# Kernel tuning notes

Hardware: AMD Instinct MI355X
Metric: run time of the kernel (lower is better)

## Reference

```python
import jax, jax.numpy as jnp
import numpy as np

EPS_W = 1e-8   # weight reciprocal eps (matches torch code)
EPS_BN = 1e-5  # torch BatchNorm1d default eps


def _cdist(a, b):
    # a: [B,N,3], b: [B,M,3] -> [B,N,M] euclidean distances
    sq = (jnp.sum(a * a, -1)[:, :, None] + jnp.sum(b * b, -1)[:, None, :]
          - 2.0 * jnp.einsum('bnd,bmd->bnm', a, b))
    return jnp.sqrt(jnp.maximum(sq, 0.0))


def _bn_relu(x, gamma, beta):
    # x: [B,C,N]; training-mode batch norm over (B,N)
    mean = jnp.mean(x, axis=(0, 2), keepdims=True)
    var = jnp.mean((x - mean) ** 2, axis=(0, 2), keepdims=True)
    y = (x - mean) * jax.lax.rsqrt(var + EPS_BN)
    y = y * gamma[None, :, None] + beta[None, :, None]
    return jax.nn.relu(y)


def setup_inputs() -> dict:
    key = jax.random.key(0)
    ks = jax.random.split(key, 8)
    B, Np, Ns = 16, 1024, 4096
    Cp, Cs, Co = 256, 128, 256
    return {
        'xyz_prev': jax.random.normal(ks[0], (B, Np, 3), jnp.float32),
        'xyz_skip': jax.random.normal(ks[1], (B, Ns, 3), jnp.float32),
        'points_prev': jax.random.normal(ks[2], (B, Cp, Np), jnp.float32),
        'points_skip': jax.random.normal(ks[3], (B, Cs, Ns), jnp.float32),
        'W1': jax.random.normal(ks[4], (Co, Cp + Cs), jnp.float32) * 0.05,
        'g1': jnp.ones((Co,), jnp.float32),
        'b1': jnp.zeros((Co,), jnp.float32),
        'W2': jax.random.normal(ks[5], (Co, Co), jnp.float32) * 0.05,
        'g2': jnp.ones((Co,), jnp.float32),
        'b2': jnp.zeros((Co,), jnp.float32),
    }


def reference(xyz_prev, xyz_skip, points_prev, points_skip, W1, g1, b1, W2, g2, b2):
    dist = _cdist(xyz_skip, xyz_prev)                       # [B,Ns,Np]
    neg, idx = jax.lax.top_k(-dist, 3)                      # 3 smallest dists
    dist_recip = 1.0 / (dist + EPS_W)
    # NOTE: normalization is over ALL N_prev points (faithful to source)
    weight = dist_recip / jnp.sum(dist_recip, axis=2, keepdims=True)
    w3 = jnp.take_along_axis(weight, idx, axis=2)           # [B,Ns,3]
    pp = jnp.swapaxes(points_prev, 1, 2)                    # [B,Np,Cp]
    g = jnp.take_along_axis(pp[:, None, :, :], idx[..., None], axis=2)  # [B,Ns,3,Cp]
    interp = jnp.einsum('bnk,bnkc->bcn', w3, g)             # [B,Cp,Ns]
    x = jnp.concatenate([interp, points_skip], axis=1)      # [B,Cp+Cs,Ns]
    x = _bn_relu(jnp.einsum('bcn,oc->bon', x, W1), g1, b1)
    x = _bn_relu(jnp.einsum('bcn,oc->bon', x, W2), g2, b2)
    return x
```

## Files before the change

### kernel.cpp

```cpp
#include <hip/hip_runtime.h>
#include <math.h>

constexpr int NB  = 16;
constexpr int NP  = 1024;
constexpr int NS  = 4096;
constexpr int CP  = 256;
constexpr int CS  = 128;
constexpr int CIN = 384;
constexpr int CO  = 256;

constexpr int NCHUNK = 16;
constexpr int CHPTS  = NP / NCHUNK;

typedef unsigned int uint;
typedef unsigned short ushort_t;
typedef __attribute__((ext_vector_type(8))) short short8;
typedef __attribute__((ext_vector_type(8))) unsigned short us8;
typedef __attribute__((ext_vector_type(4))) float f32x4;

__device__ __forceinline__ ushort_t f2bf(float f) {
  uint u = __float_as_uint(f);
  uint r = (u + 0x7fffu + ((u >> 16) & 1u)) >> 16;
  return (ushort_t)r;
}
__device__ __forceinline__ float bf2f(ushort_t u) {
  return __uint_as_float(((uint)u) << 16);
}

__device__ __forceinline__ void gload16(const void* g, void* l) {
  __builtin_amdgcn_global_load_lds(
      (const __attribute__((address_space(1))) uint*)g,
      (__attribute__((address_space(3))) uint*)l, 16, 0, 0);
}

__device__ __forceinline__ void tkp(float pxv, float pyv, float pzv, int pi,
                                    float qx, float qy, float qz,
                                    float& k0, float& k1, float& k2,
                                    float& rsum) {
  float dx = pxv - qx, dy = pyv - qy, dz = pzv - qz;
  float sq = fmaf(dz, dz, fmaf(dy, dy, fmaf(dx, dx, 1e-16f)));
  rsum += __builtin_amdgcn_rsqf(sq);
  float k = __uint_as_float((__float_as_uint(sq) & 0xFFFFFC00u) | (uint)pi);
  k2 = __builtin_amdgcn_fmed3f(k1, k2, k);
  k1 = __builtin_amdgcn_fmed3f(k0, k1, k);
  k0 = fminf(k0, k);
}

__global__ __launch_bounds__(256) void topk_chunk_kernel(
    const float* __restrict__ xyz_prev, const float* __restrict__ xyz_skip,
    float* __restrict__ pbuf) {
  __shared__ float px[CHPTS], py[CHPTS], pz[CHPTS];
  int q  = blockIdx.y;
  int b  = blockIdx.z;
  int tid = threadIdx.x;
  if (tid < CHPTS) {
    const float* xp = xyz_prev + ((size_t)b * NP + q * CHPTS + tid) * 3;
    px[tid] = xp[0]; py[tid] = xp[1]; pz[tid] = xp[2];
  }
  __syncthreads();
  int nA = blockIdx.x * 512 + tid;
  int nB = nA + 256;
  const float* xqA = xyz_skip + ((size_t)b * NS + nA) * 3;
  const float* xqB = xyz_skip + ((size_t)b * NS + nB) * 3;
  float qxA = xqA[0], qyA = xqA[1], qzA = xqA[2];
  float qxB = xqB[0], qyB = xqB[1], qzB = xqB[2];
  float kA0 = INFINITY, kA1 = INFINITY, kA2 = INFINITY;
  float kB0 = INFINITY, kB1 = INFINITY, kB2 = INFINITY;
  float rsA = 0.f, rsB = 0.f;
  int pbase = q * CHPTS;
  for (int p = 0; p < CHPTS; p += 4) {
    float4 X = *(const float4*)&px[p];
    float4 Y = *(const float4*)&py[p];
    float4 Z = *(const float4*)&pz[p];
    tkp(X.x, Y.x, Z.x, pbase + p + 0, qxA, qyA, qzA, kA0, kA1, kA2, rsA);
    tkp(X.x, Y.x, Z.x, pbase + p + 0, qxB, qyB, qzB, kB0, kB1, kB2, rsB);
    tkp(X.y, Y.y, Z.y, pbase + p + 1, qxA, qyA, qzA, kA0, kA1, kA2, rsA);
    tkp(X.y, Y.y, Z.y, pbase + p + 1, qxB, qyB, qzB, kB0, kB1, kB2, rsB);
    tkp(X.z, Y.z, Z.z, pbase + p + 2, qxA, qyA, qzA, kA0, kA1, kA2, rsA);
    tkp(X.z, Y.z, Z.z, pbase + p + 2, qxB, qyB, qzB, kB0, kB1, kB2, rsB);
    tkp(X.w, Y.w, Z.w, pbase + p + 3, qxA, qyA, qzA, kA0, kA1, kA2, rsA);
    tkp(X.w, Y.w, Z.w, pbase + p + 3, qxB, qyB, qzB, kB0, kB1, kB2, rsB);
  }
  size_t PA = ((size_t)(b * NCHUNK + q) * NS + nA) * 4;
  size_t PB = ((size_t)(b * NCHUNK + q) * NS + nB) * 4;
  *(float4*)(pbuf + PA) = make_float4(kA0, kA1, kA2, rsA);
  *(float4*)(pbuf + PB) = make_float4(kB0, kB1, kB2, rsB);
}

__global__ __launch_bounds__(256) void topk_merge_kernel(
    const float* __restrict__ pbuf, float* __restrict__ w3,
    int* __restrict__ idx3) {
  int gid = blockIdx.x * 256 + threadIdx.x;
  int b = gid >> 12;
  int n = gid & (NS - 1);
  float k0 = INFINITY, k1 = INFINITY, k2 = INFINITY;
  float rsum = 0.f;
  #pragma unroll 4
  for (int q = 0; q < NCHUNK; q++) {
    float4 v = *(const float4*)(pbuf + ((size_t)(b * NCHUNK + q) * NS + n) * 4);
    rsum += v.w;
    k2 = __builtin_amdgcn_fmed3f(k1, k2, v.x);
    k1 = __builtin_amdgcn_fmed3f(k0, k1, v.x);
    k0 = fminf(k0, v.x);
    k2 = __builtin_amdgcn_fmed3f(k1, k2, v.y);
    k1 = __builtin_amdgcn_fmed3f(k0, k1, v.y);
    k0 = fminf(k0, v.y);
    k2 = __builtin_amdgcn_fmed3f(k1, k2, v.z);
    k1 = __builtin_amdgcn_fmed3f(k0, k1, v.z);
    k0 = fminf(k0, v.z);
  }
  float inv = 1.0f / rsum;
  uint u0 = __float_as_uint(k0), u1 = __float_as_uint(k1), u2 = __float_as_uint(k2);
  float d0 = __uint_as_float(u0 & 0xFFFFFC00u);
  float d1 = __uint_as_float(u1 & 0xFFFFFC00u);
  float d2 = __uint_as_float(u2 & 0xFFFFFC00u);
  size_t base = (size_t)gid * 3;
  w3[base + 0] = __builtin_amdgcn_rsqf(d0) * inv;
  w3[base + 1] = __builtin_amdgcn_rsqf(d1) * inv;
  w3[base + 2] = __builtin_amdgcn_rsqf(d2) * inv;
  idx3[base + 0] = (int)(u0 & 1023u);
  idx3[base + 1] = (int)(u1 & 1023u);
  idx3[base + 2] = (int)(u2 & 1023u);
}

__global__ __launch_bounds__(256) void wcast_kernel(
    const float* __restrict__ W1, const float* __restrict__ W2,
    ushort_t* __restrict__ W1b, ushort_t* __restrict__ W2b,
    float* __restrict__ st1, float* __restrict__ st2) {
  int tid = threadIdx.x;
  if (blockIdx.x == 0) {
    st1[tid] = 0.f; st1[tid + 256] = 0.f;
    st2[tid] = 0.f; st2[tid + 256] = 0.f;
  }
  int t = blockIdx.x * 256 + tid;
  int n1 = CO * CIN / 4;
  if (t < n1) {
    float4 v = *(const float4*)(W1 + t * 4);
    ushort4 o; o.x = f2bf(v.x); o.y = f2bf(v.y); o.z = f2bf(v.z); o.w = f2bf(v.w);
    *(ushort4*)(W1b + t * 4) = o;
  } else {
    int u = t - n1;
    float4 v = *(const float4*)(W2 + u * 4);
    ushort4 o; o.x = f2bf(v.x); o.y = f2bf(v.y); o.z = f2bf(v.z); o.w = f2bf(v.w);
    *(ushort4*)(W2b + u * 4) = o;
  }
}

__global__ __launch_bounds__(256) void ppT_kernel(
    const float* __restrict__ pp, ushort_t* __restrict__ pptT) {
  __shared__ float tl[64][65];
  int p0 = blockIdx.x * 64, c0 = blockIdx.y * 64, b = blockIdx.z;
  int tid = threadIdx.x;
  const float* P = pp + (size_t)b * CP * NP;
  int pi4 = (tid & 15) * 4, ci = tid >> 4;
  #pragma unroll
  for (int r = 0; r < 4; r++) {
    int cc = ci + 16 * r;
    float4 v = *(const float4*)(P + (size_t)(c0 + cc) * NP + p0 + pi4);
    tl[cc][pi4] = v.x; tl[cc][pi4 + 1] = v.y; tl[cc][pi4 + 2] = v.z; tl[cc][pi4 + 3] = v.w;
  }
  __syncthreads();
  ushort_t* O = pptT + (size_t)b * NP * CP;
  int ci4 = (tid & 15) * 4, pi = tid >> 4;
  #pragma unroll
  for (int r = 0; r < 4; r++) {
    int pr = pi + 16 * r;
    ushort4 o;
    o.x = f2bf(tl[ci4 + 0][pr]); o.y = f2bf(tl[ci4 + 1][pr]);
    o.z = f2bf(tl[ci4 + 2][pr]); o.w = f2bf(tl[ci4 + 3][pr]);
    *(ushort4*)(O + (size_t)(p0 + pr) * CP + c0 + ci4) = o;
  }
}

__global__ __launch_bounds__(256) void skipT_kernel(
    const float* __restrict__ sk, ushort_t* __restrict__ x1) {
  __shared__ float tl[64][65];
  int n0 = blockIdx.x * 64, c0 = blockIdx.y * 64, b = blockIdx.z;
  int tid = threadIdx.x;
  const float* S = sk + (size_t)b * CS * NS;
  int ni4 = (tid & 15) * 4, ci = tid >> 4;
  #pragma unroll
  for (int r = 0; r < 4; r++) {
    int cc = ci + 16 * r;
    float4 v = *(const float4*)(S + (size_t)(c0 + cc) * NS + n0 + ni4);
    tl[cc][ni4] = v.x; tl[cc][ni4 + 1] = v.y; tl[cc][ni4 + 2] = v.z; tl[cc][ni4 + 3] = v.w;
  }
  __syncthreads();
  ushort_t* O = x1 + (size_t)b * NS * CIN;
  int ci4 = (tid & 15) * 4, ni = tid >> 4;
  #pragma unroll
  for (int r = 0; r < 4; r++) {
    int nr = ni + 16 * r;
    ushort4 o;
    o.x = f2bf(tl[ci4 + 0][nr]); o.y = f2bf(tl[ci4 + 1][nr]);
    o.z = f2bf(tl[ci4 + 2][nr]); o.w = f2bf(tl[ci4 + 3][nr]);
    *(ushort4*)(O + (size_t)(n0 + nr) * CIN + CP + c0 + ci4) = o;
  }
}

__global__ __launch_bounds__(256) void interp_kernel(
    const ushort_t* __restrict__ pptT, const float* __restrict__ w3,
    const int* __restrict__ idx3, ushort_t* __restrict__ x1) {
  int tid = threadIdx.x;
  int nl = tid >> 6, l = tid & 63;
  int b = blockIdx.y;
  int n = blockIdx.x * 4 + nl;
  size_t nb = (size_t)b * NS + n;
  int j0 = idx3[nb * 3 + 0], j1 = idx3[nb * 3 + 1], j2 = idx3[nb * 3 + 2];
  float w0 = w3[nb * 3 + 0], w1 = w3[nb * 3 + 1], w2 = w3[nb * 3 + 2];
  const ushort_t* P = pptT + (size_t)b * NP * CP;
  int c = l * 4;
  ushort4 g0 = *(const ushort4*)(P + (size_t)j0 * CP + c);
  ushort4 g1 = *(const ushort4*)(P + (size_t)j1 * CP + c);
  ushort4 g2 = *(const ushort4*)(P + (size_t)j2 * CP + c);
  ushort4 o;
  o.x = f2bf(w0 * bf2f(g0.x) + w1 * bf2f(g1.x) + w2 * bf2f(g2.x));
  o.y = f2bf(w0 * bf2f(g0.y) + w1 * bf2f(g1.y) + w2 * bf2f(g2.y));
  o.z = f2bf(w0 * bf2f(g0.z) + w1 * bf2f(g1.z) + w2 * bf2f(g2.z));
  o.w = f2bf(w0 * bf2f(g0.w) + w1 * bf2f(g1.w) + w2 * bf2f(g2.w));
  *(ushort4*)(x1 + nb * CIN + c) = o;
}

template <int MODE>
__global__ __launch_bounds__(256, 4) void gemm_bk64_kernel(
    const ushort_t* __restrict__ X, const ushort_t* __restrict__ Wb,
    ushort_t* __restrict__ Yb, float* __restrict__ stats,
    const float* __restrict__ stats_in, const float* __restrict__ g_in,
    const float* __restrict__ bt_in) {
  constexpr int KD = MODE ? CO : CIN;
  constexpr int NT = KD / 64;
  __shared__ __align__(16) char lds_raw[33792];
  ushort_t* ldsX = (ushort_t*)lds_raw;
  ushort_t* ldsW = (ushort_t*)(lds_raw + 16384);
  __shared__ float ssum[128], ssq[128];
  __shared__ float a1s[MODE ? CO : 1], s1s[MODE ? CO : 1];

  int tid = threadIdx.x;
  int w = tid >> 6, l = tid & 63;
  int bid = blockIdx.x;
  int by = (bid >> 3) & 1;
  int s = (bid & 7) + 8 * (bid >> 4);
  int bx = s & 31, bz = s >> 5;
  int n0 = bx * 128;
  if (tid < 128) { ssum[tid] = 0.f; ssq[tid] = 0.f; }
  if constexpr (MODE == 1) {
    float cnt = (float)NB * (float)NS;
    float m = stats_in[tid] / cnt;
    float var = stats_in[CO + tid] / cnt - m * m;
    var = fmaxf(var, 0.f);
    float invs = rsqrtf(var + 1e-5f);
    float av = g_in[tid] * invs;
    a1s[tid] = av; s1s[tid] = bt_in[tid] - m * av;
  }
  __syncthreads();

  int grow = l >> 3;
  int glc  = (l & 7) ^ grow;
  int trow = tid >> 3;
  int tlc  = (tid & 7) ^ (trow & 7);
  const ushort_t* Xb = X + (size_t)bz * NS * KD;

  f32x4 acc[4][4];
  #pragma unroll
  for (int i = 0; i < 4; i++)
    #pragma unroll
    for (int j = 0; j < 4; j++) acc[i][j] = {0.f, 0.f, 0.f, 0.f};

  int wn = (w & 1) * 64, wo = (w >> 1) * 64;
  int lr = l & 15, lk = l >> 4;

  for (int t = 0; t < NT; t++) {
    int k0 = t * 64;
    #pragma unroll
    for (int i = 0; i < 4; i++) {
      int row = w * 32 + i * 8 + grow;
      gload16(Wb + (size_t)(by * 128 + row) * KD + k0 + glc * 8,
              &ldsW[(w * 32 + i * 8) * 64]);
    }
    if constexpr (MODE == 0) {
      #pragma unroll
      for (int i = 0; i < 4; i++) {
        int row = w * 32 + i * 8 + grow;
        gload16(Xb + (size_t)(n0 + row) * KD + k0 + glc * 8,
                &ldsX[(w * 32 + i * 8) * 64]);
      }
    } else {
      #pragma unroll
      for (int c = 0; c < 4; c++) {
        int row = trow + 32 * c;
        us8 v = *(const us8*)(Xb + (size_t)(n0 + row) * KD + k0 + tlc * 8);
        const float* ap = &a1s[k0 + tlc * 8];
        const float* sp = &s1s[k0 + tlc * 8];
        us8 o;
        #pragma unroll
        for (int e = 0; e < 8; e++)
          o[e] = f2bf(fmaxf(fmaf(ap[e], bf2f(v[e]), sp[e]), 0.f));
        *(us8*)&ldsX[(tid + 256 * c) * 8] = o;
      }
    }
    __syncthreads();
    #pragma unroll
    for (int ks = 0; ks < 2; ks++) {
      short8 af[4], bfr[4];
      #pragma unroll
      for (int i = 0; i < 4; i++) {
        int rr = wn + i * 16 + lr;
        int pc = (ks * 4 + lk) ^ (rr & 7);
        af[i] = *(const short8*)&ldsX[rr * 64 + pc * 8];
      }
      #pragma unroll
      for (int j = 0; j < 4; j++) {
        int rr = wo + j * 16 + lr;
        int pc = (ks * 4 + lk) ^ (rr & 7);
        bfr[j] = *(const short8*)&ldsW[rr * 64 + pc * 8];
      }
      __builtin_amdgcn_s_setprio(1);
      #pragma unroll
      for (int i = 0; i < 4; i++)
        #pragma unroll
        for (int j = 0; j < 4; j++)
          acc[i][j] = __builtin_amdgcn_mfma_f32_16x16x32_bf16(af[i], bfr[j], acc[i][j], 0, 0, 0);
      __builtin_amdgcn_s_setprio(0);
    }
    __syncthreads();
  }

  #pragma unroll
  for (int j = 0; j < 4; j++) {
    int ol = wo + j * 16 + lr;
    float ps = 0.f, pq = 0.f;
    #pragma unroll
    for (int i = 0; i < 4; i++)
      #pragma unroll
      for (int rg = 0; rg < 4; rg++) { float v = acc[i][j][rg]; ps += v; pq += v * v; }
    atomicAdd(&ssum[ol], ps);
    atomicAdd(&ssq[ol], pq);
  }
  ushort_t* lout = (ushort_t*)lds_raw;
  #pragma unroll
  for (int i = 0; i < 4; i++)
    #pragma unroll
    for (int j = 0; j < 4; j++)
      #pragma unroll
      for (int rg = 0; rg < 4; rg++) {
        int nl = wn + i * 16 + lk * 4 + rg;
        int ol = wo + j * 16 + lr;
        lout[nl * 132 + ol] = f2bf(acc[i][j][rg]);
      }
  __syncthreads();
  {
    int row = tid >> 1, half = tid & 1;
    const ushort_t* src = lout + row * 132 + half * 64;
    ushort_t* dst = Yb + ((size_t)bz * NS + n0 + row) * CO + by * 128 + half * 64;
    #pragma unroll
    for (int k = 0; k < 8; k++)
      *(us8*)(dst + k * 8) = *(const us8*)(src + k * 8);
  }
  if (tid < 128) {
    atomicAdd(&stats[by * 128 + tid], ssum[tid]);
    atomicAdd(&stats[CO + by * 128 + tid], ssq[tid]);
  }
}

__global__ __launch_bounds__(256) void bnrelu_tr_kernel(
    const ushort_t* __restrict__ y2b, const float* __restrict__ stats_in,
    const float* __restrict__ g_in, const float* __restrict__ bt_in,
    float* __restrict__ out) {
  __shared__ float tl[64][65];
  __shared__ float a2s[64], s2s[64];
  int n0 = blockIdx.x * 64, o0 = blockIdx.y * 64, b = blockIdx.z;
  const ushort_t* Y = y2b + (size_t)b * NS * CO;
  int tid = threadIdx.x;
  if (tid < 64) {
    int o = o0 + tid;
    float cnt = (float)NB * (float)NS;
    float m = stats_in[o] / cnt;
    float var = stats_in[CO + o] / cnt - m * m;
    var = fmaxf(var, 0.f);
    float invs = rsqrtf(var + 1e-5f);
    float av = g_in[o] * invs;
    a2s[tid] = av; s2s[tid] = bt_in[o] - m * av;
  }
  int o8 = (tid & 7) * 8, row = tid >> 3;
  #pragma unroll
  for (int r = 0; r < 2; r++) {
    int ii = row + 32 * r;
    const ushort_t* src = Y + (size_t)(n0 + ii) * CO + o0 + o8;
    ushort4 v0 = *(const ushort4*)(src);
    ushort4 v1 = *(const ushort4*)(src + 4);
    tl[ii][o8 + 0] = bf2f(v0.x); tl[ii][o8 + 1] = bf2f(v0.y);
    tl[ii][o8 + 2] = bf2f(v0.z); tl[ii][o8 + 3] = bf2f(v0.w);
    tl[ii][o8 + 4] = bf2f(v1.x); tl[ii][o8 + 5] = bf2f(v1.y);
    tl[ii][o8 + 6] = bf2f(v1.z); tl[ii][o8 + 7] = bf2f(v1.w);
  }
  __syncthreads();
  float* O = out + (size_t)b * CO * NS;
  int ii4 = (tid & 15) * 4, j = tid >> 4;
  #pragma unroll
  for (int r = 0; r < 4; r++) {
    int jj = j + 16 * r;
    float av = a2s[jj], sv = s2s[jj];
    float4 v;
    v.x = fmaxf(fmaf(av, tl[ii4 + 0][jj], sv), 0.f);
    v.y = fmaxf(fmaf(av, tl[ii4 + 1][jj], sv), 0.f);
    v.z = fmaxf(fmaf(av, tl[ii4 + 2][jj], sv), 0.f);
    v.w = fmaxf(fmaf(av, tl[ii4 + 3][jj], sv), 0.f);
    *(float4*)(O + (size_t)(o0 + jj) * NS + n0 + ii4) = v;
  }
}

extern "C" void kernel_launch(void* const* d_in, const int* in_sizes, int n_in,
                              void* d_out, int out_size, void* d_ws, size_t ws_size,
                              hipStream_t stream) {
  const float* xyz_prev    = (const float*)d_in[0];
  const float* xyz_skip    = (const float*)d_in[1];
  const float* points_prev = (const float*)d_in[2];
  const float* points_skip = (const float*)d_in[3];
  const float* W1 = (const float*)d_in[4];
  const float* g1 = (const float*)d_in[5];
  const float* b1 = (const float*)d_in[6];
  const float* W2 = (const float*)d_in[7];
  const float* g2 = (const float*)d_in[8];
  const float* b2 = (const float*)d_in[9];
  float* out = (float*)d_out;

  char* W = (char*)d_ws;
  size_t off = 0;
  auto alloc = [&](size_t bytes) {
    size_t o = off; off = (off + bytes + 255) & ~(size_t)255; return o;
  };
  ushort_t* x1   = (ushort_t*)(W + alloc((size_t)NB * NS * CIN * 2));
  ushort_t* y1b  = (ushort_t*)(W + alloc((size_t)NB * NS * CO * 2));
  ushort_t* pptT = (ushort_t*)(W + alloc((size_t)NB * NP * CP * 2));
  ushort_t* W1b  = (ushort_t*)(W + alloc((size_t)CO * CIN * 2));
  ushort_t* W2b  = (ushort_t*)(W + alloc((size_t)CO * CO * 2));
  float* w3   = (float*)(W + alloc((size_t)NB * NS * 3 * 4));
  int*   idx3 = (int*)(W + alloc((size_t)NB * NS * 3 * 4));
  float* st1  = (float*)(W + alloc(512 * 4));
  float* st2  = (float*)(W + alloc(512 * 4));
  size_t y2_off = alloc((size_t)NB * NS * CO * 2);
  bool full = (ws_size >= off);
  ushort_t* y2b = full ? (ushort_t*)(W + y2_off) : (ushort_t*)d_out;
  float* pbuf = full ? (float*)(W + y2_off) : (float*)d_out;

  hipLaunchKernelGGL(topk_chunk_kernel, dim3(NS / 512, NCHUNK, NB), dim3(256), 0,
                     stream, xyz_prev, xyz_skip, pbuf);
  hipLaunchKernelGGL(topk_merge_kernel, dim3(NB * NS / 256), dim3(256), 0, stream,
                     pbuf, w3, idx3);
  hipLaunchKernelGGL(wcast_kernel, dim3((CO * CIN / 4 + CO * CO / 4 + 255) / 256),
                     dim3(256), 0, stream, W1, W2, W1b, W2b, st1, st2);
  hipLaunchKernelGGL(ppT_kernel, dim3(NP / 64, CP / 64, NB), dim3(256), 0, stream,
                     points_prev, pptT);
  hipLaunchKernelGGL(skipT_kernel, dim3(NS / 64, CS / 64, NB), dim3(256), 0, stream,
                     points_skip, x1);
  hipLaunchKernelGGL(interp_kernel, dim3(NS / 4, NB), dim3(256), 0, stream,
                     pptT, w3, idx3, x1);
  hipLaunchKernelGGL((gemm_bk64_kernel<0>), dim3(1024), dim3(256), 0, stream,
                     x1, W1b, y1b, st1, (const float*)nullptr,
                     (const float*)nullptr, (const float*)nullptr);
  hipLaunchKernelGGL((gemm_bk64_kernel<1>), dim3(1024), dim3(256), 0, stream,
                     y1b, W2b, y2b, st2, st1, g1, b1);
  if (full) {
    hipLaunchKernelGGL(bnrelu_tr_kernel, dim3(NS / 64, CO / 64, NB), dim3(256), 0,
                       stream, y2b, st2, g2, b2, out);
  } else {
    float* stage = (float*)d_ws;
    hipLaunchKernelGGL(bnrelu_tr_kernel, dim3(NS / 64, CO / 64, NB), dim3(256), 0,
                       stream, y2b, st2, g2, b2, stage);
    hipMemcpyAsync(out, stage, (size_t)NB * NS * CO * 4, hipMemcpyDeviceToDevice,
                   stream);
  }
}
```

Baseline: 165.8 us.

## Double-buffer LDS tiles in BN-fused GEMM to overlap loads with MFMA

Converts the GEMM main loop to a double-buffered LDS pipeline. The next K-tile's W and X loads, or in mode 1 the BN+ReLU activation write, are issued before the current tile's MFMAs, and mode 1 keeps register-prefetched X two tiles ahead. One barrier per iteration replaces the previous two __syncthreads, with explicit waitcnt and sched barriers. LDS usage doubles to 64KB and launch bounds drop to 2 blocks per CU, trading occupancy for latency hiding. The hand-tuned vmcnt counts are fragile if the compiler reorders the loads.

```diff
diff --git a/kernel.cpp b/kernel.cpp
--- a/kernel.cpp
+++ b/kernel.cpp
@@ -222,16 +222,14 @@
 }
 
 template <int MODE>
-__global__ __launch_bounds__(256, 4) void gemm_bk64_kernel(
+__global__ __launch_bounds__(256, 2) void gemm_bk64_kernel(
     const ushort_t* __restrict__ X, const ushort_t* __restrict__ Wb,
     ushort_t* __restrict__ Yb, float* __restrict__ stats,
     const float* __restrict__ stats_in, const float* __restrict__ g_in,
     const float* __restrict__ bt_in) {
   constexpr int KD = MODE ? CO : CIN;
   constexpr int NT = KD / 64;
-  __shared__ __align__(16) char lds_raw[33792];
-  ushort_t* ldsX = (ushort_t*)lds_raw;
-  ushort_t* ldsW = (ushort_t*)(lds_raw + 16384);
+  __shared__ __align__(16) char lds_raw[65536];
   __shared__ float ssum[128], ssq[128];
   __shared__ float a1s[MODE ? CO : 1], s1s[MODE ? CO : 1];
 
@@ -260,69 +258,126 @@
   int tlc  = (tid & 7) ^ (trow & 7);
   const ushort_t* Xb = X + (size_t)bz * NS * KD;
 
-  f32x4 acc[4][4];
-  #pragma unroll
-  for (int i = 0; i < 4; i++)
-    #pragma unroll
-    for (int j = 0; j < 4; j++) acc[i][j] = {0.f, 0.f, 0.f, 0.f};
-
-  int wn = (w & 1) * 64, wo = (w >> 1) * 64;
-  int lr = l & 15, lk = l >> 4;
-
-  for (int t = 0; t < NT; t++) {
+  auto ldsXp = [&](int buf) { return (ushort_t*)(lds_raw + buf * 16384); };
+  auto ldsWp = [&](int buf) { return (ushort_t*)(lds_raw + 32768 + buf * 16384); };
+
+  auto stageW = [&](int t, int buf) {
     int k0 = t * 64;
+    ushort_t* dW = ldsWp(buf);
     #pragma unroll
     for (int i = 0; i < 4; i++) {
       int row = w * 32 + i * 8 + grow;
       gload16(Wb + (size_t)(by * 128 + row) * KD + k0 + glc * 8,
-              &ldsW[(w * 32 + i * 8) * 64]);
+              &dW[(w * 32 + i * 8) * 64]);
     }
-    if constexpr (MODE == 0) {
-      #pragma unroll
-      for (int i = 0; i < 4; i++) {
-        int row = w * 32 + i * 8 + grow;
-        gload16(Xb + (size_t)(n0 + row) * KD + k0 + glc * 8,
-                &ldsX[(w * 32 + i * 8) * 64]);
-      }
-    } else {
+  };
+  auto stageX0 = [&](int t, int buf) {
+    int k0 = t * 64;
+    ushort_t* dX = ldsXp(buf);
+    #pragma unroll
+    for (int i = 0; i < 4; i++) {
+      int row = w * 32 + i * 8 + grow;
+      gload16(Xb + (size_t)(n0 + row) * KD + k0 + glc * 8,
+              &dX[(w * 32 + i * 8) * 64]);
+    }
+  };
+
+  us8 xr[2][4];
+  auto issueXreg = [&](int t) {
+    if constexpr (MODE == 1) {
+      int k0 = t * 64, sl = t & 1;
       #pragma unroll
       for (int c = 0; c < 4; c++) {
         int row = trow + 32 * c;
-        us8 v = *(const us8*)(Xb + (size_t)(n0 + row) * KD + k0 + tlc * 8);
-        const float* ap = &a1s[k0 + tlc * 8];
-        const float* sp = &s1s[k0 + tlc * 8];
+        xr[sl][c] = *(const us8*)(Xb + (size_t)(n0 + row) * KD + k0 + tlc * 8);
+      }
+    }
+  };
+  auto writeact = [&](int t, int buf) {
+    if constexpr (MODE == 1) {
+      int k0 = t * 64, sl = t & 1;
+      ushort_t* dX = ldsXp(buf);
+      const float* ap = &a1s[k0 + tlc * 8];
+      const float* sp = &s1s[k0 + tlc * 8];
+      #pragma unroll
+      for (int c = 0; c < 4; c++) {
+        us8 v = xr[sl][c];
         us8 o;
         #pragma unroll
         for (int e = 0; e < 8; e++)
           o[e] = f2bf(fmaxf(fmaf(ap[e], bf2f(v[e]), sp[e]), 0.f));
-        *(us8*)&ldsX[(tid + 256 * c) * 8] = o;
+        *(us8*)&dX[(tid + 256 * c) * 8] = o;
       }
     }
-    __syncthreads();
+  };
+
+  f32x4 acc[4][4];
+  #pragma unroll
+  for (int i = 0; i < 4; i++)
     #pragma unroll
-    for (int ks = 0; ks < 2; ks++) {
-      short8 af[4], bfr[4];
+    for (int j = 0; j < 4; j++) acc[i][j] = {0.f, 0.f, 0.f, 0.f};
+
+  int wn = (w & 1) * 64, wo = (w >> 1) * 64;
+  int lr = l & 15, lk = l >> 4;
+
+  if constexpr (MODE == 0) {
+    stageW(0, 0); stageX0(0, 0);
+    asm volatile("s_waitcnt vmcnt(0)" ::: "memory");
+  } else {
+    issueXreg(0);
+    stageW(0, 0);
+    issueXreg(1);
+    writeact(0, 0);
+    asm volatile("s_waitcnt vmcnt(2) lgkmcnt(0)" ::: "memory");
+  }
+  __builtin_amdgcn_s_barrier();
+  __builtin_amdgcn_sched_barrier(0);
+
+  int cur = 0;
+  #pragma unroll
+  for (int t = 0; t < NT; t++) {
+    if (t + 1 < NT) {
+      stageW(t + 1, cur ^ 1);
+      if constexpr (MODE == 0) stageX0(t + 1, cur ^ 1);
+      else writeact(t + 1, cur ^ 1);
+    }
+    if constexpr (MODE == 1) { if (t + 2 < NT) issueXreg(t + 2); }
+    {
+      const ushort_t* cX = ldsXp(cur);
+      const ushort_t* cW = ldsWp(cur);
       #pragma unroll
-      for (int i = 0; i < 4; i++) {
-        int rr = wn + i * 16 + lr;
-        int pc = (ks * 4 + lk) ^ (rr & 7);
-        af[i] = *(const short8*)&ldsX[rr * 64 + pc * 8];
+      for (int ks = 0; ks < 2; ks++) {
+        short8 af[4], bfr[4];
+        #pragma unroll
+        for (int i = 0; i < 4; i++) {
+          int rr = wn + i * 16 + lr;
+          int pc = (ks * 4 + lk) ^ (rr & 7);
+          af[i] = *(const short8*)&cX[rr * 64 + pc * 8];
+        }
+        #pragma unroll
+        for (int j = 0; j < 4; j++) {
+          int rr = wo + j * 16 + lr;
+          int pc = (ks * 4 + lk) ^ (rr & 7);
+          bfr[j] = *(const short8*)&cW[rr * 64 + pc * 8];
+        }
+        asm volatile("s_waitcnt lgkmcnt(0)" ::: "memory");
+        __builtin_amdgcn_sched_barrier(0);
+        __builtin_amdgcn_s_setprio(1);
+        #pragma unroll
+        for (int i = 0; i < 4; i++)
+          #pragma unroll
+          for (int j = 0; j < 4; j++)
+            acc[i][j] = __builtin_amdgcn_mfma_f32_16x16x32_bf16(af[i], bfr[j], acc[i][j], 0, 0, 0);
+        __builtin_amdgcn_s_setprio(0);
       }
-      #pragma unroll
-      for (int j = 0; j < 4; j++) {
-        int rr = wo + j * 16 + lr;
-        int pc = (ks * 4 + lk) ^ (rr & 7);
-        bfr[j] = *(const short8*)&ldsW[rr * 64 + pc * 8];
-      }
-      __builtin_amdgcn_s_setprio(1);
-      #pragma unroll
-      for (int i = 0; i < 4; i++)
-        #pragma unroll
-        for (int j = 0; j < 4; j++)
-          acc[i][j] = __builtin_amdgcn_mfma_f32_16x16x32_bf16(af[i], bfr[j], acc[i][j], 0, 0, 0);
-      __builtin_amdgcn_s_setprio(0);
     }
-    __syncthreads();
+    if (MODE == 1 && t + 2 < NT)
+      asm volatile("s_waitcnt vmcnt(2) lgkmcnt(0)" ::: "memory");
+    else
+      asm volatile("s_waitcnt vmcnt(0) lgkmcnt(0)" ::: "memory");
+    __builtin_amdgcn_s_barrier();
+    __builtin_amdgcn_sched_barrier(0);
+    cur ^= 1;
   }
 
   #pragma unroll
```

New measurement: 163.2 us. Within noise of the previous version (-1.6%).

## Fuse interpolation gather into first GEMM and cover all output channels per block

Applied to the files above, without the earlier changes.

Removes the separate interp kernel and the materialised x1 buffer: the first GEMM now gathers the three neighbour rows from pptT, weights them and reads the skip features directly while staging its X tile into LDS. Each block grows to 512 threads and computes all 256 output channels for 128 points, so every X tile is loaded once instead of twice. Global stat atomics are replaced by per-block partial stats written to a buffer plus a small reduction kernel. This trades extra launches and a larger LDS footprint, which may lower occupancy, for less global traffic.

```diff
diff --git a/kernel.cpp b/kernel.cpp
--- a/kernel.cpp
+++ b/kernel.cpp
@@ -173,7 +173,7 @@
 }
 
 __global__ __launch_bounds__(256) void skipT_kernel(
-    const float* __restrict__ sk, ushort_t* __restrict__ x1) {
+    const float* __restrict__ sk, ushort_t* __restrict__ xsk) {
   __shared__ float tl[64][65];
   int n0 = blockIdx.x * 64, c0 = blockIdx.y * 64, b = blockIdx.z;
   int tid = threadIdx.x;
@@ -186,7 +186,7 @@
     tl[cc][ni4] = v.x; tl[cc][ni4 + 1] = v.y; tl[cc][ni4 + 2] = v.z; tl[cc][ni4 + 3] = v.w;
   }
   __syncthreads();
-  ushort_t* O = x1 + (size_t)b * NS * CIN;
+  ushort_t* O = xsk + (size_t)b * NS * CS;
   int ci4 = (tid & 15) * 4, ni = tid >> 4;
   #pragma unroll
   for (int r = 0; r < 4; r++) {
@@ -194,71 +194,74 @@
     ushort4 o;
     o.x = f2bf(tl[ci4 + 0][nr]); o.y = f2bf(tl[ci4 + 1][nr]);
     o.z = f2bf(tl[ci4 + 2][nr]); o.w = f2bf(tl[ci4 + 3][nr]);
-    *(ushort4*)(O + (size_t)(n0 + nr) * CIN + CP + c0 + ci4) = o;
-  }
-}
-
-__global__ __launch_bounds__(256) void interp_kernel(
-    const ushort_t* __restrict__ pptT, const float* __restrict__ w3,
-    const int* __restrict__ idx3, ushort_t* __restrict__ x1) {
-  int tid = threadIdx.x;
-  int nl = tid >> 6, l = tid & 63;
-  int b = blockIdx.y;
-  int n = blockIdx.x * 4 + nl;
-  size_t nb = (size_t)b * NS + n;
-  int j0 = idx3[nb * 3 + 0], j1 = idx3[nb * 3 + 1], j2 = idx3[nb * 3 + 2];
-  float w0 = w3[nb * 3 + 0], w1 = w3[nb * 3 + 1], w2 = w3[nb * 3 + 2];
-  const ushort_t* P = pptT + (size_t)b * NP * CP;
-  int c = l * 4;
-  ushort4 g0 = *(const ushort4*)(P + (size_t)j0 * CP + c);
-  ushort4 g1 = *(const ushort4*)(P + (size_t)j1 * CP + c);
-  ushort4 g2 = *(const ushort4*)(P + (size_t)j2 * CP + c);
-  ushort4 o;
-  o.x = f2bf(w0 * bf2f(g0.x) + w1 * bf2f(g1.x) + w2 * bf2f(g2.x));
-  o.y = f2bf(w0 * bf2f(g0.y) + w1 * bf2f(g1.y) + w2 * bf2f(g2.y));
-  o.z = f2bf(w0 * bf2f(g0.z) + w1 * bf2f(g1.z) + w2 * bf2f(g2.z));
-  o.w = f2bf(w0 * bf2f(g0.w) + w1 * bf2f(g1.w) + w2 * bf2f(g2.w));
-  *(ushort4*)(x1 + nb * CIN + c) = o;
+    *(ushort4*)(O + (size_t)(n0 + nr) * CS + c0 + ci4) = o;
+  }
+}
+
+__global__ __launch_bounds__(512) void statreduce_kernel(
+    const float* __restrict__ pstat, float* __restrict__ stats) {
+  int t = threadIdx.x;
+  int r0 = blockIdx.x * 32;
+  float a = 0.f;
+  #pragma unroll
+  for (int i = 0; i < 32; i++) a += pstat[(size_t)(r0 + i) * 512 + t];
+  atomicAdd(&stats[t], a);
 }
 
 template <int MODE>
-__global__ __launch_bounds__(256, 4) void gemm_bk64_kernel(
-    const ushort_t* __restrict__ X, const ushort_t* __restrict__ Wb,
-    ushort_t* __restrict__ Yb, float* __restrict__ stats,
+__global__ __launch_bounds__(512, 4) void gemm_fco_kernel(
+    const ushort_t* __restrict__ Xsrc,
+    const ushort_t* __restrict__ xsk,
+    const float* __restrict__ w3, const int* __restrict__ idx3,
+    const ushort_t* __restrict__ Wb, ushort_t* __restrict__ Yb,
+    float* __restrict__ pstat,
     const float* __restrict__ stats_in, const float* __restrict__ g_in,
     const float* __restrict__ bt_in) {
   constexpr int KD = MODE ? CO : CIN;
   constexpr int NT = KD / 64;
-  __shared__ __align__(16) char lds_raw[33792];
+  __shared__ __align__(16) char lds_raw[49152];
   ushort_t* ldsX = (ushort_t*)lds_raw;
   ushort_t* ldsW = (ushort_t*)(lds_raw + 16384);
-  __shared__ float ssum[128], ssq[128];
+  __shared__ float ssum[CO], ssq[CO];
   __shared__ float a1s[MODE ? CO : 1], s1s[MODE ? CO : 1];
 
   int tid = threadIdx.x;
   int w = tid >> 6, l = tid & 63;
   int bid = blockIdx.x;
-  int by = (bid >> 3) & 1;
-  int s = (bid & 7) + 8 * (bid >> 4);
-  int bx = s & 31, bz = s >> 5;
+  int bz = bid >> 5, bx = bid & 31;
   int n0 = bx * 128;
-  if (tid < 128) { ssum[tid] = 0.f; ssq[tid] = 0.f; }
+  if (tid < 256) { ssum[tid] = 0.f; ssq[tid] = 0.f; }
   if constexpr (MODE == 1) {
-    float cnt = (float)NB * (float)NS;
-    float m = stats_in[tid] / cnt;
-    float var = stats_in[CO + tid] / cnt - m * m;
-    var = fmaxf(var, 0.f);
-    float invs = rsqrtf(var + 1e-5f);
-    float av = g_in[tid] * invs;
-    a1s[tid] = av; s1s[tid] = bt_in[tid] - m * av;
+    if (tid < 256) {
+      float cnt = (float)NB * (float)NS;
+      float m = stats_in[tid] / cnt;
+      float var = stats_in[CO + tid] / cnt - m * m;
+      var = fmaxf(var, 0.f);
+      float invs = rsqrtf(var + 1e-5f);
+      float av = g_in[tid] * invs;
+      a1s[tid] = av; s1s[tid] = bt_in[tid] - m * av;
+    }
   }
   __syncthreads();
 
+  int xrow = tid >> 2, xh = tid & 3;
+  int xp0 = 2 * xh, xp1 = 2 * xh + 1;
+  int xl0 = xp0 ^ (xrow & 7), xl1 = xp1 ^ (xrow & 7);
   int grow = l >> 3;
   int glc  = (l & 7) ^ grow;
-  int trow = tid >> 3;
-  int tlc  = (tid & 7) ^ (trow & 7);
-  const ushort_t* Xb = X + (size_t)bz * NS * KD;
+
+  int j0 = 0, j1 = 0, j2 = 0; float w0 = 0.f, w1 = 0.f, w2 = 0.f;
+  const ushort_t* Pb = nullptr; const ushort_t* Kb = nullptr;
+  const ushort_t* Xb = nullptr;
+  if constexpr (MODE == 0) {
+    size_t nb3 = ((size_t)bz * NS + n0 + xrow) * 3;
+    j0 = idx3[nb3 + 0]; j1 = idx3[nb3 + 1]; j2 = idx3[nb3 + 2];
+    w0 = w3[nb3 + 0]; w1 = w3[nb3 + 1]; w2 = w3[nb3 + 2];
+    Pb = Xsrc + (size_t)bz * NP * CP;
+    Kb = xsk + ((size_t)bz * NS + n0 + xrow) * CS;
+  } else {
+    Xb = Xsrc + ((size_t)bz * NS + n0 + xrow) * KD;
+  }
 
   f32x4 acc[4][4];
   #pragma unroll
@@ -266,7 +269,8 @@
     #pragma unroll
     for (int j = 0; j < 4; j++) acc[i][j] = {0.f, 0.f, 0.f, 0.f};
 
-  int wn = (w & 1) * 64, wo = (w >> 1) * 64;
+  int wr = w >> 2, wc = w & 3;
+  int wn = wr * 64, wo = wc * 64;
   int lr = l & 15, lk = l >> 4;
 
   for (int t = 0; t < NT; t++) {
@@ -274,29 +278,43 @@
     #pragma unroll
     for (int i = 0; i < 4; i++) {
       int row = w * 32 + i * 8 + grow;
-      gload16(Wb + (size_t)(by * 128 + row) * KD + k0 + glc * 8,
+      gload16(Wb + (size_t)row * KD + k0 + glc * 8,
               &ldsW[(w * 32 + i * 8) * 64]);
     }
-    if constexpr (MODE == 0) {
-      #pragma unroll
-      for (int i = 0; i < 4; i++) {
-        int row = w * 32 + i * 8 + grow;
-        gload16(Xb + (size_t)(n0 + row) * KD + k0 + glc * 8,
-                &ldsX[(w * 32 + i * 8) * 64]);
+    {
+      us8 v0, v1;
+      if constexpr (MODE == 0) {
+        if (k0 < CP) {
+          us8 a0 = *(const us8*)(Pb + (size_t)j0 * CP + k0 + xl0 * 8);
+          us8 b0 = *(const us8*)(Pb + (size_t)j1 * CP + k0 + xl0 * 8);
+          us8 c0 = *(const us8*)(Pb + (size_t)j2 * CP + k0 + xl0 * 8);
+          us8 a1 = *(const us8*)(Pb + (size_t)j0 * CP + k0 + xl1 * 8);
+          us8 b1 = *(const us8*)(Pb + (size_t)j1 * CP + k0 + xl1 * 8);
+          us8 c1 = *(const us8*)(Pb + (size_t)j2 * CP + k0 + xl1 * 8);
+          #pragma unroll
+          for (int e = 0; e < 8; e++) {
+            v0[e] = f2bf(w0 * bf2f(a0[e]) + w1 * bf2f(b0[e]) + w2 * bf2f(c0[e]));
+            v1[e] = f2bf(w0 * bf2f(a1[e]) + w1 * bf2f(b1[e]) + w2 * bf2f(c1[e]));
+          }
+        } else {
+          v0 = *(const us8*)(Kb + k0 - CP + xl0 * 8);
+          v1 = *(const us8*)(Kb + k0 - CP + xl1 * 8);
+        }
+      } else {
+        us8 r0 = *(const us8*)(Xb + k0 + xl0 * 8);
+        us8 r1 = *(const us8*)(Xb + k0 + xl1 * 8);
+        const float* a0p = &a1s[k0 + xl0 * 8];
+        const float* s0p = &s1s[k0 + xl0 * 8];
+        const float* a1p = &a1s[k0 + xl1 * 8];
+        const float* s1p = &s1s[k0 + xl1 * 8];
+        #pragma unroll
+        for (int e = 0; e < 8; e++) {
+          v0[e] = f2bf(fmaxf(fmaf(a0p[e], bf2f(r0[e]), s0p[e]), 0.f));
+          v1[e] = f2bf(fmaxf(fmaf(a1p[e], bf2f(r1[e]), s1p[e]), 0.f));
+        }
       }
-    } else {
-      #pragma unroll
-      for (int c = 0; c < 4; c++) {
-        int row = trow + 32 * c;
-        us8 v = *(const us8*)(Xb + (size_t)(n0 + row) * KD + k0 + tlc * 8);
-        const float* ap = &a1s[k0 + tlc * 8];
-        const float* sp = &s1s[k0 + tlc * 8];
-        us8 o;
-        #pragma unroll
-        for (int e = 0; e < 8; e++)
-          o[e] = f2bf(fmaxf(fmaf(ap[e], bf2f(v[e]), sp[e]), 0.f));
-        *(us8*)&ldsX[(tid + 256 * c) * 8] = o;
-      }
+      *(us8*)&ldsX[xrow * 64 + xp0 * 8] = v0;
+      *(us8*)&ldsX[xrow * 64 + xp1 * 8] = v1;
     }
     __syncthreads();
     #pragma unroll
@@ -338,27 +356,34 @@
   }
   ushort_t* lout = (ushort_t*)lds_raw;
   #pragma unroll
-  for (int i = 0; i < 4; i++)
-    #pragma unroll
-    for (int j = 0; j < 4; j++)
+  for (int p = 0; p < 2; p++) {
+    if (wr == p) {
       #pragma unroll
-      for (int rg = 0; rg < 4; rg++) {
-        int nl = wn + i * 16 + lk * 4 + rg;
-        int ol = wo + j * 16 + lr;
-        lout[nl * 132 + ol] = f2bf(acc[i][j][rg]);
-      }
-  __syncthreads();
+      for (int i = 0; i < 4; i++)
+        #pragma unroll
+        for (int j = 0; j < 4; j++)
+          #pragma unroll
+          for (int rg = 0; rg < 4; rg++) {
+            int nl = i * 16 + lk * 4 + rg;
+            int ol = wo + j * 16 + lr;
+            lout[nl * 272 + ol] = f2bf(acc[i][j][rg]);
+          }
+    }
+    __syncthreads();
+    {
+      int row = tid >> 3, co = (tid & 7) * 32;
+      const ushort_t* src = lout + row * 272 + co;
+      ushort_t* dst = Yb + ((size_t)bz * NS + n0 + p * 64 + row) * CO + co;
+      #pragma unroll
+      for (int k = 0; k < 4; k++)
+        *(us8*)(dst + k * 8) = *(const us8*)(src + k * 8);
+    }
+    __syncthreads();
+  }
   {
-    int row = tid >> 1, half = tid & 1;
-    const ushort_t* src = lout + row * 132 + half * 64;
-    ushort_t* dst = Yb + ((size_t)bz * NS + n0 + row) * CO + by * 128 + half * 64;
-    #pragma unroll
-    for (int k = 0; k < 8; k++)
-      *(us8*)(dst + k * 8) = *(const us8*)(src + k * 8);
-  }
-  if (tid < 128) {
-    atomicAdd(&stats[by * 128 + tid], ssum[tid]);
-    atomicAdd(&stats[CO + by * 128 + tid], ssq[tid]);
+    float* ps = pstat + (size_t)bid * 512;
+    if (tid < 256) ps[tid] = ssum[tid];
+    else ps[256 + (tid - 256)] = ssq[tid - 256];
   }
 }
 
@@ -429,7 +454,7 @@
   auto alloc = [&](size_t bytes) {
     size_t o = off; off = (off + bytes + 255) & ~(size_t)255; return o;
   };
-  ushort_t* x1   = (ushort_t*)(W + alloc((size_t)NB * NS * CIN * 2));
+  ushort_t* xsk  = (ushort_t*)(W + alloc((size_t)NB * NS * CS * 2));
   ushort_t* y1b  = (ushort_t*)(W + alloc((size_t)NB * NS * CO * 2));
   ushort_t* pptT = (ushort_t*)(W + alloc((size_t)NB * NP * CP * 2));
   ushort_t* W1b  = (ushort_t*)(W + alloc((size_t)CO * CIN * 2));
@@ -438,6 +463,8 @@
   int*   idx3 = (int*)(W + alloc((size_t)NB * NS * 3 * 4));
   float* st1  = (float*)(W + alloc(512 * 4));
   float* st2  = (float*)(W + alloc(512 * 4));
+  float* pst1 = (float*)(W + alloc(512 * 512 * 4));
+  float* pst2 = (float*)(W + alloc(512 * 512 * 4));
   size_t y2_off = alloc((size_t)NB * NS * CO * 2);
   bool full = (ws_size >= off);
   ushort_t* y2b = full ? (ushort_t*)(W + y2_off) : (ushort_t*)d_out;
@@ -452,14 +479,16 @@
   hipLaunchKernelGGL(ppT_kernel, dim3(NP / 64, CP / 64, NB), dim3(256), 0, stream,
                      points_prev, pptT);
   hipLaunchKernelGGL(skipT_kernel, dim3(NS / 64, CS / 64, NB), dim3(256), 0, stream,
-                     points_skip, x1);
-  hipLaunchKernelGGL(interp_kernel, dim3(NS / 4, NB), dim3(256), 0, stream,
-                     pptT, w3, idx3, x1);
-  hipLaunchKernelGGL((gemm_bk64_kernel<0>), dim3(1024), dim3(256), 0, stream,
-                     x1, W1b, y1b, st1, (const float*)nullptr,
-                     (const float*)nullptr, (const float*)nullptr);
-  hipLaunchKernelGGL((gemm_bk64_kernel<1>), dim3(1024), dim3(256), 0, stream,
-                     y1b, W2b, y2b, st2, st1, g1, b1);
+                     points_skip, xsk);
+  hipLaunchKernelGGL((gemm_fco_kernel<0>), dim3(512), dim3(512), 0, stream,
+                     pptT, xsk, w3, idx3, W1b, y1b, pst1,
+                     (const float*)nullptr, (const float*)nullptr,
+                     (const float*)nullptr);
+  hipLaunchKernelGGL(statreduce_kernel, dim3(16), dim3(512), 0, stream, pst1, st1);
+  hipLaunchKernelGGL((gemm_fco_kernel<1>), dim3(512), dim3(512), 0, stream,
+                     y1b, (const ushort_t*)nullptr, (const float*)nullptr,
+                     (const int*)nullptr, W2b, y2b, pst2, st1, g1, b1);
+  hipLaunchKernelGGL(statreduce_kernel, dim3(16), dim3(512), 0, stream, pst2, st2);
   if (full) {
     hipLaunchKernelGGL(bnrelu_tr_kernel, dim3(NS / 64, CO / 64, NB), dim3(256), 0,
                        stream, y2b, st2, g2, b2, out);
```

After: 169.9 us. 1.02x slower.

## Retile GEMMs to 32-row by full-CO tiles with per-block stat partials

Applied to the files above, without the earlier changes.

Each GEMM block now computes all 256 output channels for 32 points with a K step of 32 instead of a 128x128 tile with K step 64. That doubles the grid to 2048 blocks and cuts LDS use, so more blocks can be resident at once. Per-block BN statistics are written to a partial buffer and summed by a new reduction kernel, replacing global float atomics. The trade-off is lower reuse of the weight tile per block, more W reloads from L2, more barriers per K loop, and two extra kernel launches.

```diff
diff --git a/kernel.cpp b/kernel.cpp
--- a/kernel.cpp
+++ b/kernel.cpp
@@ -221,28 +221,36 @@
   *(ushort4*)(x1 + nb * CIN + c) = o;
 }
 
+__global__ __launch_bounds__(512) void statreduce_kernel(
+    const float* __restrict__ pstat, float* __restrict__ stats) {
+  int t = threadIdx.x;
+  int r0 = blockIdx.x * 32;
+  float a = 0.f;
+  #pragma unroll
+  for (int i = 0; i < 32; i++) a += pstat[(size_t)(r0 + i) * 512 + t];
+  atomicAdd(&stats[t], a);
+}
+
 template <int MODE>
-__global__ __launch_bounds__(256, 4) void gemm_bk64_kernel(
+__global__ __launch_bounds__(256) void gemm_tlp_kernel(
     const ushort_t* __restrict__ X, const ushort_t* __restrict__ Wb,
-    ushort_t* __restrict__ Yb, float* __restrict__ stats,
+    ushort_t* __restrict__ Yb, float* __restrict__ pstat,
     const float* __restrict__ stats_in, const float* __restrict__ g_in,
     const float* __restrict__ bt_in) {
   constexpr int KD = MODE ? CO : CIN;
-  constexpr int NT = KD / 64;
-  __shared__ __align__(16) char lds_raw[33792];
+  constexpr int NT = KD / 32;
+  __shared__ __align__(16) char lds_raw[18432];
   ushort_t* ldsX = (ushort_t*)lds_raw;
-  ushort_t* ldsW = (ushort_t*)(lds_raw + 16384);
-  __shared__ float ssum[128], ssq[128];
+  ushort_t* ldsW = (ushort_t*)(lds_raw + 2048);
+  __shared__ float ssum[CO], ssq[CO];
   __shared__ float a1s[MODE ? CO : 1], s1s[MODE ? CO : 1];
 
   int tid = threadIdx.x;
   int w = tid >> 6, l = tid & 63;
   int bid = blockIdx.x;
-  int by = (bid >> 3) & 1;
-  int s = (bid & 7) + 8 * (bid >> 4);
-  int bx = s & 31, bz = s >> 5;
-  int n0 = bx * 128;
-  if (tid < 128) { ssum[tid] = 0.f; ssq[tid] = 0.f; }
+  int bz = bid >> 7, nt = bid & 127;
+  int n0 = nt * 32;
+  if (tid < 256) { ssum[tid] = 0.f; ssq[tid] = 0.f; }
   if constexpr (MODE == 1) {
     float cnt = (float)NB * (float)NS;
     float m = stats_in[tid] / cnt;
@@ -254,69 +262,66 @@
   }
   __syncthreads();
 
-  int grow = l >> 3;
-  int glc  = (l & 7) ^ grow;
-  int trow = tid >> 3;
-  int tlc  = (tid & 7) ^ (trow & 7);
   const ushort_t* Xb = X + (size_t)bz * NS * KD;
-
-  f32x4 acc[4][4];
-  #pragma unroll
-  for (int i = 0; i < 4; i++)
+  int grow = l >> 2, gph = l & 3;
+  int arow = tid >> 2, aph = tid & 3;
+  int alg = aph ^ ((arow >> 1) & 3);
+
+  f32x4 acc[2][4];
+  #pragma unroll
+  for (int i = 0; i < 2; i++)
     #pragma unroll
     for (int j = 0; j < 4; j++) acc[i][j] = {0.f, 0.f, 0.f, 0.f};
 
-  int wn = (w & 1) * 64, wo = (w >> 1) * 64;
+  int wo = w * 64;
   int lr = l & 15, lk = l >> 4;
 
   for (int t = 0; t < NT; t++) {
-    int k0 = t * 64;
+    int k0 = t * 32;
     #pragma unroll
     for (int i = 0; i < 4; i++) {
-      int row = w * 32 + i * 8 + grow;
-      gload16(Wb + (size_t)(by * 128 + row) * KD + k0 + glc * 8,
-              &ldsW[(w * 32 + i * 8) * 64]);
+      int rl = w * 64 + i * 16 + grow;
+      int lg = gph ^ ((rl >> 1) & 3);
+      gload16(Wb + (size_t)rl * KD + k0 + lg * 8,
+              &ldsW[(w * 64 + i * 16) * 32]);
     }
     if constexpr (MODE == 0) {
-      #pragma unroll
-      for (int i = 0; i < 4; i++) {
-        int row = w * 32 + i * 8 + grow;
-        gload16(Xb + (size_t)(n0 + row) * KD + k0 + glc * 8,
-                &ldsX[(w * 32 + i * 8) * 64]);
+      if (w < 2) {
+        int rl = w * 16 + grow;
+        int lg = gph ^ ((rl >> 1) & 3);
+        gload16(Xb + (size_t)(n0 + rl) * KD + k0 + lg * 8,
+                &ldsX[(w * 16) * 32]);
       }
     } else {
-      #pragma unroll
-      for (int c = 0; c < 4; c++) {
-        int row = trow + 32 * c;
-        us8 v = *(const us8*)(Xb + (size_t)(n0 + row) * KD + k0 + tlc * 8);
-        const float* ap = &a1s[k0 + tlc * 8];
-        const float* sp = &s1s[k0 + tlc * 8];
+      if (tid < 128) {
+        us8 v = *(const us8*)(Xb + (size_t)(n0 + arow) * KD + k0 + alg * 8);
+        const float* ap = &a1s[k0 + alg * 8];
+        const float* sp = &s1s[k0 + alg * 8];
         us8 o;
         #pragma unroll
         for (int e = 0; e < 8; e++)
           o[e] = f2bf(fmaxf(fmaf(ap[e], bf2f(v[e]), sp[e]), 0.f));
-        *(us8*)&ldsX[(tid + 256 * c) * 8] = o;
+        *(us8*)&ldsX[arow * 32 + aph * 8] = o;
       }
     }
     __syncthreads();
-    #pragma unroll
-    for (int ks = 0; ks < 2; ks++) {
-      short8 af[4], bfr[4];
+    {
+      short8 af[2], bfr[4];
       #pragma unroll
-      for (int i = 0; i < 4; i++) {
-        int rr = wn + i * 16 + lr;
-        int pc = (ks * 4 + lk) ^ (rr & 7);
-        af[i] = *(const short8*)&ldsX[rr * 64 + pc * 8];
+      for (int i = 0; i < 2; i++) {
+        int rr = i * 16 + lr;
+        int pc = lk ^ ((rr >> 1) & 3);
+        af[i] = *(const short8*)&ldsX[rr * 32 + pc * 8];
       }
       #pragma unroll
       for (int j = 0; j < 4; j++) {
-        int rr = wo + j * 16 + lr;
-        int pc = (ks * 4 + lk) ^ (rr & 7);
-        bfr[j] = *(const short8*)&ldsW[rr * 64 + pc * 8];
+        int rw = wo + j * 16 + lr;
+        int pc = lk ^ ((rw >> 1) & 3);
+        bfr[j] = *(const short8*)&ldsW[rw * 32 + pc * 8];
       }
       __builtin_amdgcn_s_setprio(1);
       #pragma unroll
-      for (int i = 0; i < 4; i++)
+      for (int i = 0; i < 2; i++)
         #pragma unroll
         for (int j = 0; j < 4; j++)
           acc[i][j] = __builtin_amdgcn_mfma_f32_16x16x32_bf16(af[i], bfr[j], acc[i][j], 0, 0, 0);
@@ -330,7 +335,7 @@
     int ol = wo + j * 16 + lr;
     float ps = 0.f, pq = 0.f;
     #pragma unroll
-    for (int i = 0; i < 4; i++)
+    for (int i = 0; i < 2; i++)
       #pragma unroll
       for (int rg = 0; rg < 4; rg++) { float v = acc[i][j][rg]; ps += v; pq += v * v; }
     atomicAdd(&ssum[ol], ps);
@@ -338,27 +343,28 @@
   }
   ushort_t* lout = (ushort_t*)lds_raw;
   #pragma unroll
-  for (int i = 0; i < 4; i++)
+  for (int i = 0; i < 2; i++)
     #pragma unroll
     for (int j = 0; j < 4; j++)
       #pragma unroll
       for (int rg = 0; rg < 4; rg++) {
-        int nl = wn + i * 16 + lk * 4 + rg;
+        int nl = i * 16 + lk * 4 + rg;
         int ol = wo + j * 16 + lr;
-        lout[nl * 132 + ol] = f2bf(acc[i][j][rg]);
+        lout[nl * 264 + ol] = f2bf(acc[i][j][rg]);
       }
   __syncthreads();
   {
-    int row = tid >> 1, half = tid & 1;
-    const ushort_t* src = lout + row * 132 + half * 64;
-    ushort_t* dst = Yb + ((size_t)bz * NS + n0 + row) * CO + by * 128 + half * 64;
+    int row = tid >> 3, co = (tid & 7) * 32;
+    const ushort_t* src = lout + row * 264 + co;
+    ushort_t* dst = Yb + ((size_t)bz * NS + n0 + row) * CO + co;
     #pragma unroll
-    for (int k = 0; k < 8; k++)
+    for (int k = 0; k < 4; k++)
       *(us8*)(dst + k * 8) = *(const us8*)(src + k * 8);
   }
-  if (tid < 128) {
-    atomicAdd(&stats[by * 128 + tid], ssum[tid]);
-    atomicAdd(&stats[CO + by * 128 + tid], ssq[tid]);
+  {
+    float* ps = pstat + (size_t)bid * 512;
+    ps[tid] = ssum[tid];
+    ps[256 + tid] = ssq[tid];
   }
 }
 
@@ -438,6 +444,8 @@
   int*   idx3 = (int*)(W + alloc((size_t)NB * NS * 3 * 4));
   float* st1  = (float*)(W + alloc(512 * 4));
   float* st2  = (float*)(W + alloc(512 * 4));
+  float* pst1 = (float*)(W + alloc(2048 * 512 * 4));
+  float* pst2 = (float*)(W + alloc(2048 * 512 * 4));
   size_t y2_off = alloc((size_t)NB * NS * CO * 2);
   bool full = (ws_size >= off);
   ushort_t* y2b = full ? (ushort_t*)(W + y2_off) : (ushort_t*)d_out;
@@ -455,11 +463,13 @@
                      points_skip, x1);
   hipLaunchKernelGGL(interp_kernel, dim3(NS / 4, NB), dim3(256), 0, stream,
                      pptT, w3, idx3, x1);
-  hipLaunchKernelGGL((gemm_bk64_kernel<0>), dim3(1024), dim3(256), 0, stream,
-                     x1, W1b, y1b, st1, (const float*)nullptr,
+  hipLaunchKernelGGL((gemm_tlp_kernel<0>), dim3(2048), dim3(256), 0, stream,
+                     x1, W1b, y1b, pst1, (const float*)nullptr,
                      (const float*)nullptr, (const float*)nullptr);
-  hipLaunchKernelGGL((gemm_bk64_kernel<1>), dim3(1024), dim3(256), 0, stream,
-                     y1b, W2b, y2b, st2, st1, g1, b1);
+  hipLaunchKernelGGL(statreduce_kernel, dim3(64), dim3(512), 0, stream, pst1, st1);
+  hipLaunchKernelGGL((gemm_tlp_kernel<1>), dim3(2048), dim3(256), 0, stream,
+                     y1b, W2b, y2b, pst2, st1, g1, b1);
+  hipLaunchKernelGGL(statreduce_kernel, dim3(64), dim3(512), 0, stream, pst2, st2);
   if (full) {
     hipLaunchKernelGGL(bnrelu_tr_kernel, dim3(NS / 64, CO / 64, NB), dim3(256), 0,
                        stream, y2b, st2, g2, b2, out);
```

Measured after the change: 198.9 us. 1.2x slower.
